# Kernel tuning notes

Hardware: AMD Instinct MI355X
Metric: run time of the kernel (lower is better)

Reference implementation:

```python
import jax, jax.numpy as jnp
import numpy as np

HID = 1024
VOCAB = 50257
MAXLEN = 2048


def setup_inputs() -> dict:
    key = jax.random.key(0)
    ks = jax.random.split(key, 12)
    s = 0.02
    return {
        "input_tok": jax.random.randint(ks[0], (1,), 0, VOCAB),
        "hidden": jax.random.normal(ks[1], (1, 1, HID), jnp.float32),
        "encoder_outputs": jax.random.normal(ks[2], (MAXLEN, HID), jnp.float32),
        "emb": jax.random.normal(ks[3], (VOCAB, HID), jnp.float32) * s,
        "attn_W": jax.random.normal(ks[4], (MAXLEN, 2 * HID), jnp.float32) * s,
        "attn_b": jnp.zeros((MAXLEN,), jnp.float32),
        "comb_W": jax.random.normal(ks[5], (HID, 2 * HID), jnp.float32) * s,
        "comb_b": jnp.zeros((HID,), jnp.float32),
        "W_ih": jax.random.normal(ks[6], (3 * HID, HID), jnp.float32) * s,
        "W_hh": jax.random.normal(ks[7], (3 * HID, HID), jnp.float32) * s,
        "b_ih": jnp.zeros((3 * HID,), jnp.float32),
        "b_hh": jnp.zeros((3 * HID,), jnp.float32),
        "out_W": jax.random.normal(ks[8], (VOCAB, HID), jnp.float32) * s,
        "out_b": jnp.zeros((VOCAB,), jnp.float32),
    }


def reference(input_tok, hidden, encoder_outputs, emb, attn_W, attn_b,
              comb_W, comb_b, W_ih, W_hh, b_ih, b_hh, out_W, out_b):
    H = hidden.shape[-1]
    # embedding lookup -> [1, H]; dropout is identity in eval mode
    embedded = emb[input_tok].reshape(1, H)
    h = hidden[0]  # [1, H]
    # Bahdanau-style attention over fixed max_length
    attn_weights = jax.nn.softmax(
        jnp.concatenate([embedded, h], axis=1) @ attn_W.T + attn_b, axis=1)  # [1, L]
    attn_applied = attn_weights @ encoder_outputs  # [1, H]
    x = jnp.concatenate([embedded, attn_applied], axis=1) @ comb_W.T + comb_b
    x = jax.nn.relu(x)  # [1, H]
    # single GRU step (PyTorch gate layout: r, z, n)
    gi = x @ W_ih.T + b_ih
    gh = h @ W_hh.T + b_hh
    gi_r, gi_z, gi_n = jnp.split(gi, 3, axis=1)
    gh_r, gh_z, gh_n = jnp.split(gh, 3, axis=1)
    r = jax.nn.sigmoid(gi_r + gh_r)
    z = jax.nn.sigmoid(gi_z + gh_z)
    n = jnp.tanh(gi_n + r * gh_n)
    h_new = (1.0 - z) * n + z * h  # [1, H]
    out = jax.nn.log_softmax(h_new @ out_W.T + out_b, axis=1)  # [1, V]
    return out, h_new[None], attn_weights
```

## Files before the change

### kernel.cpp

```cpp
#include <hip/hip_runtime.h>
#include <math.h>

#define HID    1024
#define VOCAB  50257
#define MAXLEN 2048
#define LOGIT_BLOCKS ((VOCAB + 3) / 4)
#define SMB 128
#define SMR (MAXLEN / SMB)

#define WS_SCORES    0
#define WS_APPLIED   4096
#define WS_X         5120
#define WS_GI        6144
#define WS_GH        9216
#define WS_HNEW      12288
#define WS_LSE       13313
#define WS_PM        16384
#define WS_PS        30720
#define WS_PARTIALS  49152

__device__ inline float wave_reduce_sum(float v) {
    #pragma unroll
    for (int m = 32; m > 0; m >>= 1) v += __shfl_xor(v, m, 64);
    return v;
}

__global__ __launch_bounds__(256) void k_attn_scores(
        const float* __restrict__ emb, const int* __restrict__ tok,
        const float* __restrict__ hidden,
        const float* __restrict__ attn_W, const float* __restrict__ attn_b,
        float* __restrict__ scores) {
    int gtid = blockIdx.x * blockDim.x + threadIdx.x;
    int row = gtid >> 6, lane = gtid & 63;
    if (row >= MAXLEN) return;
    const float* erow = emb + (size_t)tok[0] * HID;
    const float* wrow = attn_W + (size_t)row * (2 * HID);
    float acc = 0.f;
    #pragma unroll
    for (int i = 0; i < 8; ++i) {
        int k = i * 256 + lane * 4;
        float4 w = *(const float4*)(wrow + k);
        float4 c = (k < HID) ? *(const float4*)(erow + k)
                             : *(const float4*)(hidden + (k - HID));
        acc += w.x * c.x + w.y * c.y + w.z * c.z + w.w * c.w;
    }
    acc = wave_reduce_sum(acc);
    if (lane == 0) scores[row] = acc + attn_b[row];
}

__global__ __launch_bounds__(256) void k_softmax_apply(
        const float* __restrict__ scores, const float* __restrict__ E,
        float* __restrict__ out_w, float* __restrict__ partials) {
    __shared__ float red[256];
    __shared__ float wrow[SMR];
    int t = threadIdx.x, b = blockIdx.x;
    float v[8];
    float m = -INFINITY;
    #pragma unroll
    for (int i = 0; i < 8; ++i) { v[i] = scores[t + 256 * i]; m = fmaxf(m, v[i]); }
    red[t] = m; __syncthreads();
    for (int s = 128; s > 0; s >>= 1) { if (t < s) red[t] = fmaxf(red[t], red[t + s]); __syncthreads(); }
    float M = red[0]; __syncthreads();
    float s = 0.f;
    #pragma unroll
    for (int i = 0; i < 8; ++i) s += expf(v[i] - M);
    red[t] = s; __syncthreads();
    for (int k = 128; k > 0; k >>= 1) { if (t < k) red[t] += red[t + k]; __syncthreads(); }
    float invS = 1.f / red[0];
    int r0 = b * SMR;
    if (t < SMR) wrow[t] = expf(scores[r0 + t] - M) * invS;
    __syncthreads();
    int j = t * 4;
    float4 acc = make_float4(0.f, 0.f, 0.f, 0.f);
    for (int r = 0; r < SMR; ++r) {
        float w = wrow[r];
        float4 e = *(const float4*)(E + (size_t)(r0 + r) * HID + j);
        acc.x += w * e.x; acc.y += w * e.y; acc.z += w * e.z; acc.w += w * e.w;
    }
    *(float4*)(partials + (size_t)b * HID + j) = acc;
    if (b == 0) {
        #pragma unroll
        for (int i = 0; i < 8; ++i) out_w[t + 256 * i] = expf(v[i] - M) * invS;
    }
}

__global__ __launch_bounds__(256) void k_apply_reduce(
        const float* __restrict__ partials, float* __restrict__ applied) {
    int j = blockIdx.x * blockDim.x + threadIdx.x;
    float acc = 0.f;
    for (int c = 0; c < SMB; ++c) acc += partials[(size_t)c * HID + j];
    applied[j] = acc;
}

__global__ __launch_bounds__(256) void k_comb(
        const float* __restrict__ emb, const int* __restrict__ tok,
        const float* __restrict__ applied,
        const float* __restrict__ comb_W, const float* __restrict__ comb_b,
        float* __restrict__ x) {
    int gtid = blockIdx.x * blockDim.x + threadIdx.x;
    int row = gtid >> 6, lane = gtid & 63;
    if (row >= HID) return;
    const float* erow = emb + (size_t)tok[0] * HID;
    const float* wrow = comb_W + (size_t)row * (2 * HID);
    float acc = 0.f;
    #pragma unroll
    for (int i = 0; i < 8; ++i) {
        int k = i * 256 + lane * 4;
        float4 w = *(const float4*)(wrow + k);
        float4 c = (k < HID) ? *(const float4*)(erow + k)
                             : *(const float4*)(applied + (k - HID));
        acc += w.x * c.x + w.y * c.y + w.z * c.z + w.w * c.w;
    }
    acc = wave_reduce_sum(acc);
    if (lane == 0) x[row] = fmaxf(acc + comb_b[row], 0.f);
}

__global__ __launch_bounds__(256) void k_gru_gemv(
        const float* __restrict__ W_ih, const float* __restrict__ W_hh,
        const float* __restrict__ b_ih, const float* __restrict__ b_hh,
        const float* __restrict__ x, const float* __restrict__ h,
        float* __restrict__ gi, float* __restrict__ gh) {
    int gtid = blockIdx.x * blockDim.x + threadIdx.x;
    int row = gtid >> 6, lane = gtid & 63;
    if (row >= 6 * HID) return;
    const float* wrow; const float* vec;
    if (row < 3 * HID) { wrow = W_ih + (size_t)row * HID; vec = x; }
    else               { wrow = W_hh + (size_t)(row - 3 * HID) * HID; vec = h; }
    float acc = 0.f;
    #pragma unroll
    for (int i = 0; i < 4; ++i) {
        int k = i * 256 + lane * 4;
        float4 w = *(const float4*)(wrow + k);
        float4 c = *(const float4*)(vec + k);
        acc += w.x * c.x + w.y * c.y + w.z * c.z + w.w * c.w;
    }
    acc = wave_reduce_sum(acc);
    if (lane == 0) {
        if (row < 3 * HID) gi[row] = acc + b_ih[row];
        else               gh[row - 3 * HID] = acc + b_hh[row - 3 * HID];
    }
}

__global__ __launch_bounds__(256) void k_gru_gate(
        const float* __restrict__ gi, const float* __restrict__ gh,
        const float* __restrict__ h,
        float* __restrict__ hnew_out, float* __restrict__ hnew_ws) {
    int i = blockIdx.x * blockDim.x + threadIdx.x;
    float r = 1.f / (1.f + expf(-(gi[i] + gh[i])));
    float z = 1.f / (1.f + expf(-(gi[i + HID] + gh[i + HID])));
    float n = tanhf(gi[i + 2 * HID] + r * gh[i + 2 * HID]);
    float hn = (1.f - z) * n + z * h[i];
    hnew_out[i] = hn;
    hnew_ws[i]  = hn;
}

__global__ __launch_bounds__(256) void k_logits(
        const float* __restrict__ hnew, const float* __restrict__ out_W,
        const float* __restrict__ out_b,
        float* __restrict__ logits, float* __restrict__ pm, float* __restrict__ ps) {
    __shared__ float wl[4];
    int wib = threadIdx.x >> 6, lane = threadIdx.x & 63;
    int row = blockIdx.x * 4 + wib;
    float acc = 0.f;
    if (row < VOCAB) {
        const float* wrow = out_W + (size_t)row * HID;
        #pragma unroll
        for (int i = 0; i < 4; ++i) {
            int k = i * 256 + lane * 4;
            float4 w = *(const float4*)(wrow + k);
            float4 c = *(const float4*)(hnew + k);
            acc += w.x * c.x + w.y * c.y + w.z * c.z + w.w * c.w;
        }
        acc = wave_reduce_sum(acc);
        if (lane == 0) { acc += out_b[row]; logits[row] = acc; }
    }
    if (lane == 0) wl[wib] = (row < VOCAB) ? acc : -INFINITY;
    __syncthreads();
    if (threadIdx.x == 0) {
        float m = fmaxf(fmaxf(wl[0], wl[1]), fmaxf(wl[2], wl[3]));
        float s = expf(wl[0] - m) + expf(wl[1] - m) + expf(wl[2] - m) + expf(wl[3] - m);
        pm[blockIdx.x] = m;
        ps[blockIdx.x] = s;
    }
}

__global__ __launch_bounds__(1024) void k_lse_finalize(
        const float* __restrict__ pm, const float* __restrict__ ps,
        float* __restrict__ lse) {
    __shared__ float red[1024];
    int t = threadIdx.x;
    float m = -INFINITY;
    for (int i = t; i < LOGIT_BLOCKS; i += 1024) m = fmaxf(m, pm[i]);
    red[t] = m; __syncthreads();
    for (int s = 512; s > 0; s >>= 1) { if (t < s) red[t] = fmaxf(red[t], red[t + s]); __syncthreads(); }
    float M = red[0]; __syncthreads();
    float acc = 0.f;
    for (int i = t; i < LOGIT_BLOCKS; i += 1024) acc += ps[i] * expf(pm[i] - M);
    red[t] = acc; __syncthreads();
    for (int s = 512; s > 0; s >>= 1) { if (t < s) red[t] += red[t + s]; __syncthreads(); }
    if (t == 0) lse[0] = M + logf(red[0]);
}

__global__ __launch_bounds__(256) void k_writeout(float* __restrict__ out,
                                                  const float* __restrict__ lse) {
    int v = blockIdx.x * blockDim.x + threadIdx.x;
    if (v < VOCAB) out[v] -= lse[0];
}

extern "C" void kernel_launch(void* const* d_in, const int* in_sizes, int n_in,
                              void* d_out, int out_size, void* d_ws, size_t ws_size,
                              hipStream_t stream) {
    const int*   tok     = (const int*)d_in[0];
    const float* hidden  = (const float*)d_in[1];
    const float* E       = (const float*)d_in[2];
    const float* emb     = (const float*)d_in[3];
    const float* attn_W  = (const float*)d_in[4];
    const float* attn_b  = (const float*)d_in[5];
    const float* comb_W  = (const float*)d_in[6];
    const float* comb_b  = (const float*)d_in[7];
    const float* W_ih    = (const float*)d_in[8];
    const float* W_hh    = (const float*)d_in[9];
    const float* b_ih    = (const float*)d_in[10];
    const float* b_hh    = (const float*)d_in[11];
    const float* out_W   = (const float*)d_in[12];
    const float* out_b   = (const float*)d_in[13];

    float* out       = (float*)d_out;
    float* hnew_out  = out + VOCAB;
    float* attnw_out = out + VOCAB + HID;

    float* ws        = (float*)d_ws;
    float* scores    = ws + WS_SCORES;
    float* applied   = ws + WS_APPLIED;
    float* x         = ws + WS_X;
    float* gi        = ws + WS_GI;
    float* gh        = ws + WS_GH;
    float* hnew_ws   = ws + WS_HNEW;
    float* lse       = ws + WS_LSE;
    float* pm        = ws + WS_PM;
    float* ps        = ws + WS_PS;
    float* partials  = ws + WS_PARTIALS;

    k_attn_scores<<<MAXLEN / 4, 256, 0, stream>>>(emb, tok, hidden, attn_W, attn_b, scores);
    k_softmax_apply<<<SMB, 256, 0, stream>>>(scores, E, attnw_out, partials);
    k_apply_reduce<<<HID / 256, 256, 0, stream>>>(partials, applied);
    k_comb<<<HID / 4, 256, 0, stream>>>(emb, tok, applied, comb_W, comb_b, x);
    k_gru_gemv<<<(6 * HID) / 4, 256, 0, stream>>>(W_ih, W_hh, b_ih, b_hh, x, hidden, gi, gh);
    k_gru_gate<<<HID / 256, 256, 0, stream>>>(gi, gh, hidden, hnew_out, hnew_ws);
    k_logits<<<LOGIT_BLOCKS, 256, 0, stream>>>(hnew_ws, out_W, out_b, out, pm, ps);
    k_lse_finalize<<<1, 1024, 0, stream>>>(pm, ps, lse);
    k_writeout<<<(VOCAB + 255) / 256, 256, 0, stream>>>(out, lse);
}
```

Before: 74.25 us.

## Fuse LSE finalize into writeout, widen logits blocks, parallelize apply reduce

Merges the single-block log-sum-exp finalize and the writeout into one kernel. Each block now recomputes the global max and sum from the per-block partials, so one launch and the serial single-block stage go away. The logits kernel uses 512-thread blocks that process two rows per wave, which gives 16 rows per block and fewer partials. The attention softmax uses twice as many blocks, and the partial-sum reduce is now a wave-shuffle reduction with one block per column. The cost is redundant reduction work in every writeout block, which reads the whole partials array.

```diff
diff --git a/kernel.cpp b/kernel.cpp
--- a/kernel.cpp
+++ b/kernel.cpp
@@ -4,9 +4,10 @@
 #define HID    1024
 #define VOCAB  50257
 #define MAXLEN 2048
-#define LOGIT_BLOCKS ((VOCAB + 3) / 4)
-#define SMB 128
+#define SMB 256
 #define SMR (MAXLEN / SMB)
+#define LROWS 16
+#define LBLK ((VOCAB + LROWS - 1) / LROWS)
 
 #define WS_SCORES    0
 #define WS_APPLIED   4096
@@ -14,7 +15,6 @@
 #define WS_GI        6144
 #define WS_GH        9216
 #define WS_HNEW      12288
-#define WS_LSE       13313
 #define WS_PM        16384
 #define WS_PS        30720
 #define WS_PARTIALS  49152
@@ -72,6 +72,7 @@
     __syncthreads();
     int j = t * 4;
     float4 acc = make_float4(0.f, 0.f, 0.f, 0.f);
+    #pragma unroll
     for (int r = 0; r < SMR; ++r) {
         float w = wrow[r];
         float4 e = *(const float4*)(E + (size_t)(r0 + r) * HID + j);
@@ -86,10 +87,14 @@
 
 __global__ __launch_bounds__(256) void k_apply_reduce(
         const float* __restrict__ partials, float* __restrict__ applied) {
-    int j = blockIdx.x * blockDim.x + threadIdx.x;
-    float acc = 0.f;
-    for (int c = 0; c < SMB; ++c) acc += partials[(size_t)c * HID + j];
-    applied[j] = acc;
+    __shared__ float sm[4];
+    int t = threadIdx.x, j = blockIdx.x;
+    float v = partials[(size_t)t * HID + j];
+    v = wave_reduce_sum(v);
+    int wib = t >> 6, lane = t & 63;
+    if (lane == 0) sm[wib] = v;
+    __syncthreads();
+    if (t == 0) applied[j] = sm[0] + sm[1] + sm[2] + sm[3];
 }
 
 __global__ __launch_bounds__(256) void k_comb(
@@ -154,57 +159,71 @@
     hnew_ws[i]  = hn;
 }
 
-__global__ __launch_bounds__(256) void k_logits(
+__global__ __launch_bounds__(512) void k_logits(
         const float* __restrict__ hnew, const float* __restrict__ out_W,
         const float* __restrict__ out_b,
         float* __restrict__ logits, float* __restrict__ pm, float* __restrict__ ps) {
-    __shared__ float wl[4];
+    __shared__ float wm[8], wsum[8];
     int wib = threadIdx.x >> 6, lane = threadIdx.x & 63;
-    int row = blockIdx.x * 4 + wib;
-    float acc = 0.f;
-    if (row < VOCAB) {
-        const float* wrow = out_W + (size_t)row * HID;
-        #pragma unroll
-        for (int i = 0; i < 4; ++i) {
-            int k = i * 256 + lane * 4;
-            float4 w = *(const float4*)(wrow + k);
-            float4 c = *(const float4*)(hnew + k);
-            acc += w.x * c.x + w.y * c.y + w.z * c.z + w.w * c.w;
-        }
-        acc = wave_reduce_sum(acc);
-        if (lane == 0) { acc += out_b[row]; logits[row] = acc; }
-    }
-    if (lane == 0) wl[wib] = (row < VOCAB) ? acc : -INFINITY;
+    int r0 = blockIdx.x * LROWS + wib * 2;
+    bool v0 = r0 < VOCAB, v1 = (r0 + 1) < VOCAB;
+    int rr0 = v0 ? r0 : 0, rr1 = v1 ? (r0 + 1) : 0;
+    const float* w0 = out_W + (size_t)rr0 * HID;
+    const float* w1 = out_W + (size_t)rr1 * HID;
+    float acc0 = 0.f, acc1 = 0.f;
+    #pragma unroll
+    for (int i = 0; i < 4; ++i) {
+        int k = i * 256 + lane * 4;
+        float4 a = *(const float4*)(w0 + k);
+        float4 b = *(const float4*)(w1 + k);
+        float4 c = *(const float4*)(hnew + k);
+        acc0 += a.x * c.x + a.y * c.y + a.z * c.z + a.w * c.w;
+        acc1 += b.x * c.x + b.y * c.y + b.z * c.z + b.w * c.w;
+    }
+    acc0 = wave_reduce_sum(acc0);
+    acc1 = wave_reduce_sum(acc1);
+    if (lane == 0) {
+        float l0 = acc0 + out_b[rr0], l1 = acc1 + out_b[rr1];
+        if (v0) logits[r0] = l0;
+        if (v1) logits[r0 + 1] = l1;
+        float m, s;
+        if (v0 | v1) {
+            float e0 = v0 ? l0 : -INFINITY, e1 = v1 ? l1 : -INFINITY;
+            m = fmaxf(e0, e1);
+            s = (v0 ? expf(e0 - m) : 0.f) + (v1 ? expf(e1 - m) : 0.f);
+        } else { m = -INFINITY; s = 0.f; }
+        wm[wib] = m; wsum[wib] = s;
+    }
     __syncthreads();
     if (threadIdx.x == 0) {
-        float m = fmaxf(fmaxf(wl[0], wl[1]), fmaxf(wl[2], wl[3]));
-        float s = expf(wl[0] - m) + expf(wl[1] - m) + expf(wl[2] - m) + expf(wl[3] - m);
-        pm[blockIdx.x] = m;
-        ps[blockIdx.x] = s;
-    }
-}
-
-__global__ __launch_bounds__(1024) void k_lse_finalize(
+        float M = wm[0];
+        #pragma unroll
+        for (int i = 1; i < 8; ++i) M = fmaxf(M, wm[i]);
+        float S = 0.f;
+        #pragma unroll
+        for (int i = 0; i < 8; ++i) S += (wsum[i] > 0.f) ? wsum[i] * expf(wm[i] - M) : 0.f;
+        pm[blockIdx.x] = M;
+        ps[blockIdx.x] = S;
+    }
+}
+
+__global__ __launch_bounds__(256) void k_logsoftmax_write(
         const float* __restrict__ pm, const float* __restrict__ ps,
-        float* __restrict__ lse) {
-    __shared__ float red[1024];
+        float* __restrict__ out) {
+    __shared__ float red[256];
     int t = threadIdx.x;
     float m = -INFINITY;
-    for (int i = t; i < LOGIT_BLOCKS; i += 1024) m = fmaxf(m, pm[i]);
+    for (int i = t; i < LBLK; i += 256) m = fmaxf(m, pm[i]);
     red[t] = m; __syncthreads();
-    for (int s = 512; s > 0; s >>= 1) { if (t < s) red[t] = fmaxf(red[t], red[t + s]); __syncthreads(); }
+    for (int s = 128; s > 0; s >>= 1) { if (t < s) red[t] = fmaxf(red[t], red[t + s]); __syncthreads(); }
     float M = red[0]; __syncthreads();
     float acc = 0.f;
-    for (int i = t; i < LOGIT_BLOCKS; i += 1024) acc += ps[i] * expf(pm[i] - M);
+    for (int i = t; i < LBLK; i += 256) acc += ps[i] * expf(pm[i] - M);
     red[t] = acc; __syncthreads();
-    for (int s = 512; s > 0; s >>= 1) { if (t < s) red[t] += red[t + s]; __syncthreads(); }
-    if (t == 0) lse[0] = M + logf(red[0]);
-}
-
-__global__ __launch_bounds__(256) void k_writeout(float* __restrict__ out,
-                                                  const float* __restrict__ lse) {
-    int v = blockIdx.x * blockDim.x + threadIdx.x;
-    if (v < VOCAB) out[v] -= lse[0];
+    for (int s = 128; s > 0; s >>= 1) { if (t < s) red[t] += red[t + s]; __syncthreads(); }
+    float lse = M + logf(red[0]);
+    int v = blockIdx.x * 256 + t;
+    if (v < VOCAB) out[v] -= lse;
 }
 
 extern "C" void kernel_launch(void* const* d_in, const int* in_sizes, int n_in,
@@ -236,18 +255,16 @@
     float* gi        = ws + WS_GI;
     float* gh        = ws + WS_GH;
     float* hnew_ws   = ws + WS_HNEW;
-    float* lse       = ws + WS_LSE;
     float* pm        = ws + WS_PM;
     float* ps        = ws + WS_PS;
     float* partials  = ws + WS_PARTIALS;
 
     k_attn_scores<<<MAXLEN / 4, 256, 0, stream>>>(emb, tok, hidden, attn_W, attn_b, scores);
     k_softmax_apply<<<SMB, 256, 0, stream>>>(scores, E, attnw_out, partials);
-    k_apply_reduce<<<HID / 256, 256, 0, stream>>>(partials, applied);
+    k_apply_reduce<<<HID, 256, 0, stream>>>(partials, applied);
     k_comb<<<HID / 4, 256, 0, stream>>>(emb, tok, applied, comb_W, comb_b, x);
     k_gru_gemv<<<(6 * HID) / 4, 256, 0, stream>>>(W_ih, W_hh, b_ih, b_hh, x, hidden, gi, gh);
     k_gru_gate<<<HID / 256, 256, 0, stream>>>(gi, gh, hidden, hnew_out, hnew_ws);
-    k_logits<<<LOGIT_BLOCKS, 256, 0, stream>>>(hnew_ws, out_W, out_b, out, pm, ps);
-    k_lse_finalize<<<1, 1024, 0, stream>>>(pm, ps, lse);
-    k_writeout<<<(VOCAB + 255) / 256, 256, 0, stream>>>(out, lse);
-}
+    k_logits<<<LBLK, 512, 0, stream>>>(hnew_ws, out_W, out_b, out, pm, ps);
+    k_logsoftmax_write<<<(VOCAB + 255) / 256, 256, 0, stream>>>(pm, ps, out);
+}
```

New measurement: 69.27 us (median of 3 runs). -6.7%, faster.
